# Kernel tuning notes

Hardware: AMD Instinct MI355X
Metric: run time of the kernel (lower is better)

The kernel has to match this reference:

```python
import jax, jax.numpy as jnp
import numpy as np

N_GENE, N_TRAIN, E = 2500, 16384, 4194304
SRC_DIM, DST_DIM, HID, OUT, NCLS = 2500, 2675, 2500, 2500, 16


def setup_inputs() -> dict:
    key = jax.random.key(0)
    ks = jax.random.split(key, 16)
    s = 0.02
    return {
        "gene_feat": jax.random.normal(ks[0], (N_GENE, SRC_DIM), jnp.float32),
        "train_feat": jax.random.normal(ks[1], (N_TRAIN, DST_DIM), jnp.float32),
        "edge_src": jax.random.randint(ks[2], (E,), 0, N_GENE, jnp.int32),
        "edge_dst": jax.random.randint(ks[3], (E,), 0, N_TRAIN, jnp.int32),
        # conv1: SAGEConv((src=2500, dst=2675) -> 2500, mean)
        "W1_self": jax.random.normal(ks[4], (HID, DST_DIM), jnp.float32) * s,
        "W1_neigh": jax.random.normal(ks[5], (HID, SRC_DIM), jnp.float32) * s,
        "b1": jnp.zeros((HID,), jnp.float32),
        # conv2: SAGEConv(2500 -> 2500, mean); src feats are original gene feats
        "W2_self": jax.random.normal(ks[6], (OUT, HID), jnp.float32) * s,
        "W2_neigh": jax.random.normal(ks[7], (OUT, SRC_DIM), jnp.float32) * s,
        "b2": jnp.zeros((OUT,), jnp.float32),
        # classifier MLP
        "Wc1": jax.random.normal(ks[8], (OUT, OUT), jnp.float32) * s,
        "bc1": jnp.zeros((OUT,), jnp.float32),
        "Wc2": jax.random.normal(ks[9], (NCLS, OUT), jnp.float32) * s,
        "bc2": jnp.zeros((NCLS,), jnp.float32),
    }


def reference(gene_feat, train_feat, edge_src, edge_dst,
              W1_self, W1_neigh, b1, W2_self, W2_neigh, b2,
              Wc1, bc1, Wc2, bc2):
    # Dense incidence-count matrix A[dst, src]: # edges between (dst, src).
    # mean-aggregation over in-edges == (A @ gene_feat) / in_degree.
    A = jnp.zeros((N_TRAIN, N_GENE), jnp.float32).at[edge_dst, edge_src].add(1.0)
    deg = jnp.maximum(A.sum(axis=1, keepdims=True), 1.0)  # zero-in-deg -> neigh term = 0
    mean_src = (A @ gene_feat) / deg                      # [N_train, 2500]

    # conv1 ('connects'): fc_self(dst) + fc_neigh(mean(src)) + bias; then ReLU
    h = jax.nn.relu(train_feat @ W1_self.T + mean_src @ W1_neigh.T + b1)

    # conv2: dst feats = h, src feats = original gene_feat (same graph)
    h2 = jax.nn.relu(h @ W2_self.T + mean_src @ W2_neigh.T + b2)

    # classifier MLP
    return jax.nn.relu(h2 @ Wc1.T + bc1) @ Wc2.T + bc2   # [N_train, 16]
```

## Files before the change

kernel.cpp:

```cpp
#include <hip/hip_runtime.h>
#include <stdint.h>

typedef unsigned short u16;
typedef unsigned int u32;
typedef __attribute__((ext_vector_type(4))) float f32x4;
typedef __attribute__((ext_vector_type(8))) short bf16x8;

#define MROWS 16384
#define NP    2560
#define K1P   2688


__device__ __forceinline__ u16 f2bf(float f) {
    u32 u = __float_as_uint(f);
    u32 r = (u + 0x7fffu + ((u >> 16) & 1u)) >> 16;
    return (u16)r;
}

__device__ __forceinline__ void async_ld16(const void* g, void* l) {
    __builtin_amdgcn_global_load_lds((const __attribute__((address_space(1))) u32*)g,
                                     (__attribute__((address_space(3))) u32*)l,
                                     16, 0, 0);
}

__device__ __forceinline__ u32 lds_b(const void* p) {
    return (u32)(uintptr_t)(const __attribute__((address_space(3))) void*)p;
}


__global__ void cvt_pad(const float* __restrict__ src, u16* __restrict__ dst,
                        int R, int C, int Cp) {
    const int r = blockIdx.x;
    u16* drow = dst + (size_t)r * Cp;
    if (r < R) {
        const float* srow = src + (size_t)r * C;
        for (int c = threadIdx.x; c < Cp; c += blockDim.x)
            drow[c] = (c < C) ? f2bf(srow[c]) : (u16)0;
    } else {
        for (int c = threadIdx.x; c < Cp; c += blockDim.x) drow[c] = 0;
    }
}

__global__ void pad_vec(const float* __restrict__ src, float* __restrict__ dst,
                        int n, int np) {
    int i = blockIdx.x * blockDim.x + threadIdx.x;
    if (i < np) dst[i] = (i < n) ? src[i] : 0.f;
}

__global__ void transpose_cvt(const float* __restrict__ src, u16* __restrict__ dst) {
    __shared__ float t[64][65];
    const int n0 = blockIdx.x * 64;
    const int k0 = blockIdx.y * 64;
    const int tx = threadIdx.x, ty = threadIdx.y;
    for (int i = ty; i < 64; i += 4) {
        int k = k0 + i, n = n0 + tx;
        t[i][tx] = (k < 2500 && n < 2500) ? src[(size_t)k * 2500 + n] : 0.f;
    }
    __syncthreads();
    for (int i = ty; i < 64; i += 4)
        dst[(size_t)(n0 + i) * NP + k0 + tx] = f2bf(t[tx][i]);
}

__global__ void build_counts(const int* __restrict__ esrc, const int* __restrict__ edst,
                             int E, float* __restrict__ acnt) {
    int i = blockIdx.x * blockDim.x + threadIdx.x;
    if (i < E) atomicAdd(&acnt[(size_t)edst[i] * NP + esrc[i]], 1.0f);
}

__global__ void row_rdeg(const float* __restrict__ acnt, float* __restrict__ rdeg) {
    const int row = blockIdx.x;
    const float4* p = (const float4*)(acnt + (size_t)row * NP);
    float s = 0.f;
    for (int i = threadIdx.x; i < NP / 4; i += 64) {
        float4 v = p[i];
        s += v.x + v.y + v.z + v.w;
    }
    #pragma unroll
    for (int off = 32; off > 0; off >>= 1) s += __shfl_down(s, off, 64);
    if (threadIdx.x == 0) rdeg[row] = 1.f / fmaxf(s, 1.f);
}


#define DSR(dst, ad, off) \
    asm volatile("ds_read_b128 %0, %1 offset:%2" : "=v"(dst) : "v"(ad), "i"(off))

#define RD_A(SET, BUF, QM) do { \
    DSR(SET[0][0], adA0, (BUF)*32768 + (QM)*8192 + 0);    \
    DSR(SET[0][1], adA1, (BUF)*32768 + (QM)*8192 + 0);    \
    DSR(SET[1][0], adA0, (BUF)*32768 + (QM)*8192 + 2048); \
    DSR(SET[1][1], adA1, (BUF)*32768 + (QM)*8192 + 2048); \
    DSR(SET[2][0], adA0, (BUF)*32768 + (QM)*8192 + 4096); \
    DSR(SET[2][1], adA1, (BUF)*32768 + (QM)*8192 + 4096); \
    DSR(SET[3][0], adA0, (BUF)*32768 + (QM)*8192 + 6144); \
    DSR(SET[3][1], adA1, (BUF)*32768 + (QM)*8192 + 6144); \
} while (0)

#define RD_BP(SET, BUF, BASE) do { \
    DSR(SET[0][0], adB0, (BUF)*32768 + (BASE));        \
    DSR(SET[0][1], adB1, (BUF)*32768 + (BASE));        \
    DSR(SET[1][0], adB0, (BUF)*32768 + (BASE) + 2048); \
    DSR(SET[1][1], adB1, (BUF)*32768 + (BASE) + 2048); \
} while (0)

#define WAITLG(N) do { \
    asm volatile("s_waitcnt lgkmcnt(" #N ")" ::: "memory"); \
    __builtin_amdgcn_sched_barrier(0); \
} while (0)

#define MFMA_Q(QM, QN, ASET, BSET) do { \
    __builtin_amdgcn_s_setprio(1); \
    _Pragma("unroll") \
    for (int mi_ = 0; mi_ < 4; ++mi_) { \
        _Pragma("unroll") \
        for (int ni_ = 0; ni_ < 2; ++ni_) { \
            f32x4 c_ = acc[(QM)*4 + mi_][(QN)*2 + ni_]; \
            c_ = __builtin_amdgcn_mfma_f32_16x16x32_bf16(ASET[mi_][0], BSET[ni_][0], c_, 0, 0, 0); \
            c_ = __builtin_amdgcn_mfma_f32_16x16x32_bf16(ASET[mi_][1], BSET[ni_][1], c_, 0, 0, 0); \
            acc[(QM)*4 + mi_][(QN)*2 + ni_] = c_; \
        } \
    } \
    __builtin_amdgcn_s_setprio(0); \
} while (0)

#define XFEN() asm volatile("" ::: "memory")
#define XBAR() do { XFEN(); __builtin_amdgcn_s_barrier(); XFEN(); } while (0)
#define WVM4() asm volatile("s_waitcnt vmcnt(4)" ::: "memory")

template<bool PAIR2, bool BIAS_RELU>
__global__ __launch_bounds__(512, 2) void gemm256(
    const u16* __restrict__ A1, const u16* __restrict__ B1, int K1,
    const u16* __restrict__ A2, const u16* __restrict__ B2, int K2,
    const float* __restrict__ epi, u16* __restrict__ C, int N)
{
    __shared__ __align__(16) u16 lA[2 * 256 * 64];
    __shared__ __align__(16) u16 lB[2 * 256 * 64];

    const int tid  = threadIdx.x;
    const int nwg  = gridDim.x;
    const int orig = blockIdx.x;
    const int swz  = (orig & 7) * (nwg >> 3) + (orig >> 3);
    const int nt   = N >> 8;
    const int bm   = (swz / nt) << 8;
    const int bn   = (swz % nt) << 8;

    const int wave = tid >> 6, lane = tid & 63;
    const int wr   = (wave >> 2) << 7;
    const int wc   = (wave & 3) << 6;
    const int lrow = lane & 15, lkq = (lane >> 4) & 3;
    const int o0   = ((lkq ^ (lrow & 7)) << 3);

    const u32 adA0 = lds_b(lA + (wr + lrow) * 64 + o0);
    const u32 adA1 = adA0 ^ 64;
    const u32 adB0 = lds_b(lB + (wc + lrow) * 64 + o0);
    const u32 adB1 = adB0 ^ 64;

    const int sr   = tid >> 3;
    const int pc   = tid & 7;
    const int swzc = ((pc ^ (sr & 7)) << 3);
    u16* const dA  = lA + sr * 64 + pc * 8;
    u16* const dB  = lB + sr * 64 + pc * 8;

    const int nk1 = K1 >> 6;
    const int nkt = nk1 + (PAIR2 ? (K2 >> 6) : 0);

    f32x4 acc[8][4] = {};
    bf16x8 a1[4][2], a2[4][2], b23[2][2], b01A[2][2], b01B[2][2];

    auto STAGE = [&](int mat, int buf, int half, int kt) {
        int v = (kt < nkt) ? kt : kt - nkt;
        const u16* base; int K, ko;
        if (!PAIR2 || v < nk1) { base = mat ? B1 : A1; K = K1; ko = v << 6; }
        else                   { base = mat ? B2 : A2; K = K2; ko = (v - nk1) << 6; }
        const int rb = (mat ? bn : bm) + (half << 7) + sr;
        u16* d = (mat ? dB : dA) + buf * 16384 + half * 8192;
        const u16* g = base + (size_t)rb * K + ko + swzc;
        async_ld16(g, d);
        async_ld16(g + (size_t)64 * K, d + 4096);
    };

    STAGE(1, 0, 0, 0); STAGE(1, 0, 1, 0);
    STAGE(0, 0, 0, 0); STAGE(0, 0, 1, 0);
    STAGE(1, 1, 0, 1); STAGE(1, 1, 1, 1);
    WVM4();
    XBAR();
    RD_BP(b01A, 0, 0);
    RD_A(a1, 0, 0);

    const int niter = nkt >> 1;
    #pragma unroll 1
    for (int i = 0; i < niter; ++i) {
        const int t1 = 2 * i + 1, t2 = 2 * i + 2, t3 = 2 * i + 3;
        STAGE(0, 1, 0, t1);
        XBAR(); RD_BP(b23, 0, 4096); WAITLG(4); MFMA_Q(0, 0, a1, b01A); XBAR();
        STAGE(0, 1, 1, t1); WVM4();
        XBAR(); RD_A(a2, 0, 1); WAITLG(8); MFMA_Q(0, 1, a1, b23); XBAR();
        STAGE(1, 0, 0, t2);
        XBAR(); RD_BP(b01B, 1, 0); WAITLG(4); MFMA_Q(1, 1, a2, b23); XBAR();
        STAGE(1, 0, 1, t2); WVM4();
        XBAR(); RD_A(a1, 1, 0); MFMA_Q(1, 0, a2, b01A); XBAR();
        STAGE(0, 0, 0, t2);
        XBAR(); RD_BP(b23, 1, 4096); WAITLG(4); MFMA_Q(0, 0, a1, b01B); XBAR();
        STAGE(0, 0, 1, t2); WVM4();
        XBAR(); RD_A(a2, 1, 1); WAITLG(8); MFMA_Q(0, 1, a1, b23); XBAR();
        STAGE(1, 1, 0, t3);
        XBAR(); RD_BP(b01A, 0, 0); WAITLG(4); MFMA_Q(1, 1, a2, b23); XBAR();
        STAGE(1, 1, 1, t3); WVM4();
        XBAR(); RD_A(a1, 0, 0); MFMA_Q(1, 0, a2, b01B); XBAR();
    }
    asm volatile("s_waitcnt vmcnt(0) lgkmcnt(0)" ::: "memory");

    const int rbase = bm + wr + lkq * 4;
    const int cbase = bn + wc + lrow;
    if (BIAS_RELU) {
        #pragma unroll
        for (int ni = 0; ni < 4; ++ni) {
            const float bv = epi[cbase + ni * 16];
            #pragma unroll
            for (int mi = 0; mi < 8; ++mi)
                #pragma unroll
                for (int r = 0; r < 4; ++r) {
                    float v = acc[mi][ni][r] + bv;
                    v = fmaxf(v, 0.f);
                    C[(size_t)(rbase + mi * 16 + r) * N + cbase + ni * 16] = f2bf(v);
                }
        }
    } else {
        #pragma unroll
        for (int mi = 0; mi < 8; ++mi)
            #pragma unroll
            for (int r = 0; r < 4; ++r) {
                const float sv = epi[rbase + mi * 16 + r];
                #pragma unroll
                for (int ni = 0; ni < 4; ++ni)
                    C[(size_t)(rbase + mi * 16 + r) * N + cbase + ni * 16] =
                        f2bf(acc[mi][ni][r] * sv);
            }
    }
}

__device__ __forceinline__ float bfdot2(u32 a, u32 b, float acc) {
    float al = __uint_as_float(a << 16), ah = __uint_as_float(a & 0xffff0000u);
    float bl = __uint_as_float(b << 16), bh = __uint_as_float(b & 0xffff0000u);
    return fmaf(ah, bh, fmaf(al, bl, acc));
}

__global__ __launch_bounds__(256) void gemm_cls(
    const u16* __restrict__ hc, const u16* __restrict__ Wc2,
    const float* __restrict__ bc2, float* __restrict__ out)
{
    const int c = threadIdx.x & 15;
    const int r = threadIdx.x >> 4;
    const int row = blockIdx.x * 16 + r;
    const uint4* hp = (const uint4*)(hc + (size_t)row * NP);
    const uint4* wp = (const uint4*)(Wc2 + (size_t)c * NP);
    float acc = 0.f;
    #pragma unroll 4
    for (int i = 0; i < NP / 8; ++i) {
        uint4 a = hp[i], b = wp[i];
        acc = bfdot2(a.x, b.x, acc);
        acc = bfdot2(a.y, b.y, acc);
        acc = bfdot2(a.z, b.z, acc);
        acc = bfdot2(a.w, b.w, acc);
    }
    out[(size_t)row * 16 + c] = acc + bc2[c];
}


extern "C" void kernel_launch(void* const* d_in, const int* in_sizes, int n_in,
                              void* d_out, int out_size, void* d_ws, size_t ws_size,
                              hipStream_t stream) {
    const float* gene  = (const float*)d_in[0];
    const float* train = (const float*)d_in[1];
    const int*   esrc  = (const int*)d_in[2];
    const int*   edst  = (const int*)d_in[3];
    const float* W1s   = (const float*)d_in[4];
    const float* W1n   = (const float*)d_in[5];
    const float* b1    = (const float*)d_in[6];
    const float* W2s   = (const float*)d_in[7];
    const float* W2n   = (const float*)d_in[8];
    const float* b2    = (const float*)d_in[9];
    const float* Wc1   = (const float*)d_in[10];
    const float* bc1   = (const float*)d_in[11];
    const float* Wc2   = (const float*)d_in[12];
    const float* bc2   = (const float*)d_in[13];
    const int E = in_sizes[2];

    char* ws = (char*)d_ws;
    const size_t o_acnt  = 0;
    const size_t o_acntb = 167772160;
    const size_t o_mean  = 251658240;
    const size_t o_train = 335544320;
    const size_t o_w1s   = 423624704;
    const size_t o_w1n   = 437387264;
    const size_t o_w2s   = 450494464;
    const size_t o_w2n   = 463601664;
    const size_t o_wc1   = 476708864;
    const size_t o_gft   = 489816064;
    const size_t o_wc2   = 502923264;
    const size_t o_b1    = 503005184;
    const size_t o_b2    = 503015424;
    const size_t o_bc1   = 503025664;
    const size_t o_rdeg  = 503035904;

    float* ACNT = (float*)(ws + o_acnt);
    u16* ACNTB  = (u16*)(ws + o_acntb);
    u16* MEAN   = (u16*)(ws + o_mean);
    u16* TRAINB = (u16*)(ws + o_train);
    u16* W1S    = (u16*)(ws + o_w1s);
    u16* W1N    = (u16*)(ws + o_w1n);
    u16* W2S    = (u16*)(ws + o_w2s);
    u16* W2N    = (u16*)(ws + o_w2n);
    u16* WC1    = (u16*)(ws + o_wc1);
    u16* GFT    = (u16*)(ws + o_gft);
    u16* WC2    = (u16*)(ws + o_wc2);
    float* B1   = (float*)(ws + o_b1);
    float* B2   = (float*)(ws + o_b2);
    float* BC1  = (float*)(ws + o_bc1);
    float* RDEG = (float*)(ws + o_rdeg);
    u16* H  = (u16*)(ws + o_acnt);
    u16* H2 = (u16*)(ws + o_acntb);
    u16* HC = (u16*)(ws + o_mean);

    hipMemsetAsync(ACNT, 0, (size_t)MROWS * NP * 4, stream);
    build_counts<<<(E + 255) / 256, 256, 0, stream>>>(esrc, edst, E, ACNT);
    row_rdeg<<<MROWS, 64, 0, stream>>>(ACNT, RDEG);

    cvt_pad<<<MROWS, 256, 0, stream>>>(ACNT, ACNTB, MROWS, NP, NP);
    cvt_pad<<<MROWS, 256, 0, stream>>>(train, TRAINB, MROWS, 2675, K1P);
    cvt_pad<<<NP, 256, 0, stream>>>(W1s, W1S, 2500, 2675, K1P);
    cvt_pad<<<NP, 256, 0, stream>>>(W1n, W1N, 2500, 2500, NP);
    cvt_pad<<<NP, 256, 0, stream>>>(W2s, W2S, 2500, 2500, NP);
    cvt_pad<<<NP, 256, 0, stream>>>(W2n, W2N, 2500, 2500, NP);
    cvt_pad<<<NP, 256, 0, stream>>>(Wc1, WC1, 2500, 2500, NP);
    cvt_pad<<<16, 256, 0, stream>>>(Wc2, WC2, 16, 2500, NP);
    transpose_cvt<<<dim3(NP / 64, NP / 64), dim3(64, 4), 0, stream>>>(gene, GFT);
    pad_vec<<<(NP + 255) / 256, 256, 0, stream>>>(b1, B1, 2500, NP);
    pad_vec<<<(NP + 255) / 256, 256, 0, stream>>>(b2, B2, 2500, NP);
    pad_vec<<<(NP + 255) / 256, 256, 0, stream>>>(bc1, BC1, 2500, NP);

    const int NWG = (NP / 256) * (MROWS / 256);
    gemm256<false, false><<<NWG, 512, 0, stream>>>(
        ACNTB, GFT, NP, nullptr, nullptr, 0, RDEG, MEAN, NP);
    gemm256<true, true><<<NWG, 512, 0, stream>>>(
        TRAINB, W1S, K1P, MEAN, W1N, NP, B1, H, NP);
    gemm256<true, true><<<NWG, 512, 0, stream>>>(
        H, W2S, NP, MEAN, W2N, NP, B2, H2, NP);
    gemm256<false, true><<<NWG, 512, 0, stream>>>(
        H2, WC1, NP, nullptr, nullptr, 0, BC1, HC, NP);
    gemm_cls<<<MROWS / 16, 256, 0, stream>>>(HC, WC2, bc2, (float*)d_out);
}
```

Measured before the change: 2.175 ms.

## Pack edge counts into 8-bit atomics and fuse degree with bf16 conversion

```diff
diff --git a/kernel.cpp b/kernel.cpp
--- a/kernel.cpp
+++ b/kernel.cpp
@@ -61,23 +61,43 @@
         dst[(size_t)(n0 + i) * NP + k0 + tx] = f2bf(t[tx][i]);
 }
 
-__global__ void build_counts(const int* __restrict__ esrc, const int* __restrict__ edst,
-                             int E, float* __restrict__ acnt) {
+__global__ void build_counts8(const int* __restrict__ esrc, const int* __restrict__ edst,
+                              int E, u32* __restrict__ cnt) {
     int i = blockIdx.x * blockDim.x + threadIdx.x;
-    if (i < E) atomicAdd(&acnt[(size_t)edst[i] * NP + esrc[i]], 1.0f);
-}
-
-__global__ void row_rdeg(const float* __restrict__ acnt, float* __restrict__ rdeg) {
-    const int row = blockIdx.x;
-    const float4* p = (const float4*)(acnt + (size_t)row * NP);
-    float s = 0.f;
-    for (int i = threadIdx.x; i < NP / 4; i += 64) {
-        float4 v = p[i];
-        s += v.x + v.y + v.z + v.w;
-    }
+    if (i < E) {
+        u32 addr = (u32)edst[i] * NP + (u32)esrc[i];
+        atomicAdd(&cnt[addr >> 2], 1u << ((addr & 3u) * 8u));
+    }
+}
+
+__global__ void cnt_row(const u32* __restrict__ cnt, u16* __restrict__ acntb,
+                        float* __restrict__ rdeg) {
+    const int row  = blockIdx.x * 4 + (threadIdx.x >> 6);
+    const int lane = threadIdx.x & 63;
+    const uint4* src = (const uint4*)((const char*)cnt + (size_t)row * NP);
+    u16* drow = acntb + (size_t)row * NP;
+    u32 s = 0;
+    for (int i = lane; i < NP / 16; i += 64) {
+        uint4 v = src[i];
+        u32 w[4] = {v.x, v.y, v.z, v.w};
+        __align__(16) u16 o[16];
+        #pragma unroll
+        for (int j = 0; j < 4; ++j) {
+            #pragma unroll
+            for (int b = 0; b < 4; ++b) {
+                u32 byte = (w[j] >> (8 * b)) & 0xffu;
+                s += byte;
+                o[j * 4 + b] = f2bf((float)byte);
+            }
+        }
+        uint4* dst = (uint4*)(drow + i * 16);
+        dst[0] = *(const uint4*)&o[0];
+        dst[1] = *(const uint4*)&o[8];
+    }
+    float fs = (float)s;
     #pragma unroll
-    for (int off = 32; off > 0; off >>= 1) s += __shfl_down(s, off, 64);
-    if (threadIdx.x == 0) rdeg[row] = 1.f / fmaxf(s, 1.f);
+    for (int off = 32; off > 0; off >>= 1) fs += __shfl_down(fs, off, 64);
+    if (lane == 0) rdeg[row] = 1.f / fmaxf(fs, 1.f);
 }
 
 
@@ -302,7 +322,7 @@
     const size_t o_bc1   = 503025664;
     const size_t o_rdeg  = 503035904;
 
-    float* ACNT = (float*)(ws + o_acnt);
+    u32* CNT8   = (u32*)(ws + o_acnt);
     u16* ACNTB  = (u16*)(ws + o_acntb);
     u16* MEAN   = (u16*)(ws + o_mean);
     u16* TRAINB = (u16*)(ws + o_train);
@@ -321,11 +341,10 @@
     u16* H2 = (u16*)(ws + o_acntb);
     u16* HC = (u16*)(ws + o_mean);
 
-    hipMemsetAsync(ACNT, 0, (size_t)MROWS * NP * 4, stream);
-    build_counts<<<(E + 255) / 256, 256, 0, stream>>>(esrc, edst, E, ACNT);
-    row_rdeg<<<MROWS, 64, 0, stream>>>(ACNT, RDEG);
-
-    cvt_pad<<<MROWS, 256, 0, stream>>>(ACNT, ACNTB, MROWS, NP, NP);
+    hipMemsetAsync(CNT8, 0, (size_t)MROWS * NP, stream);
+    build_counts8<<<(E + 255) / 256, 256, 0, stream>>>(esrc, edst, E, CNT8);
+    cnt_row<<<MROWS / 4, 256, 0, stream>>>(CNT8, ACNTB, RDEG);
+
     cvt_pad<<<MROWS, 256, 0, stream>>>(train, TRAINB, MROWS, 2675, K1P);
     cvt_pad<<<NP, 256, 0, stream>>>(W1s, W1S, 2500, 2675, K1P);
     cvt_pad<<<NP, 256, 0, stream>>>(W1n, W1N, 2500, 2500, NP);
```

Result: faster. 2.069 ms (-4.9%).
